# Kernel optimization log

Measured on AMD Instinct MI355X. Metric: run time of the kernel, lower is better.

Reference implementation:

```python
import jax, jax.numpy as jnp
import numpy as np

B, CHAR_LEN, LSTM, VOCAB, NATTN = 4096, 64, 400, 73, 10

def _lstm_cell(x, h, c, W_ih, W_hh, b):
    # gates: [B, 4*LSTM] in (i, f, g, o) order, matching torch.nn.LSTMCell
    g = x @ W_ih.T + h @ W_hh.T + b
    i, f, gg, o = jnp.split(g, 4, axis=1)
    i = jax.nn.sigmoid(i); f = jax.nn.sigmoid(f)
    gg = jnp.tanh(gg); o = jax.nn.sigmoid(o)
    c_new = f * c + i * gg
    h_new = o * jnp.tanh(c_new)
    return h_new, c_new

def setup_inputs() -> dict:
    key = jax.random.key(0)
    ks = jax.random.split(key, 24)
    d = {}
    d['inputs'] = jax.random.normal(ks[0], (B, 3), jnp.float32)
    for n, k in zip(['h1','c1','h2','c2','h3','c3'], ks[1:7]):
        d[n] = jax.random.normal(k, (B, LSTM), jnp.float32) * 0.1
    d['kappa'] = jax.random.uniform(ks[7], (B, NATTN), jnp.float32) * 5.0
    d['w_prev'] = jax.random.uniform(ks[8], (B, VOCAB), jnp.float32)
    d['attention_values'] = jax.random.uniform(ks[9], (B, CHAR_LEN, VOCAB), jnp.float32)
    d['attention_lengths'] = jax.random.randint(ks[10], (B,), 1, CHAR_LEN + 1, jnp.int32)
    s = 0.05
    in1 = VOCAB + 3              # lstm1 input: [w, inputs]
    in23 = 3 + LSTM + VOCAB      # lstm2/3 input: [inputs, h, w]
    attn_in = VOCAB + 3 + LSTM
    d['W_ih1'] = jax.random.normal(ks[11], (4 * LSTM, in1), jnp.float32) * s
    d['W_hh1'] = jax.random.normal(ks[12], (4 * LSTM, LSTM), jnp.float32) * s
    d['b1'] = jax.random.normal(ks[13], (4 * LSTM,), jnp.float32) * s
    d['W_attn'] = jax.random.normal(ks[14], (3 * NATTN, attn_in), jnp.float32) * s
    d['b_attn'] = jax.random.normal(ks[15], (3 * NATTN,), jnp.float32) * s
    d['W_ih2'] = jax.random.normal(ks[16], (4 * LSTM, in23), jnp.float32) * s
    d['W_hh2'] = jax.random.normal(ks[17], (4 * LSTM, LSTM), jnp.float32) * s
    d['b2'] = jax.random.normal(ks[18], (4 * LSTM,), jnp.float32) * s
    d['W_ih3'] = jax.random.normal(ks[19], (4 * LSTM, in23), jnp.float32) * s
    d['W_hh3'] = jax.random.normal(ks[20], (4 * LSTM, LSTM), jnp.float32) * s
    d['b3'] = jax.random.normal(ks[21], (4 * LSTM,), jnp.float32) * s
    return d

def reference(inputs, h1, c1, h2, c2, h3, c3, kappa, w_prev, attention_values,
              attention_lengths, W_ih1, W_hh1, b1, W_attn, b_attn,
              W_ih2, W_hh2, b2, W_ih3, W_hh3, b3):
    char_len = attention_values.shape[1]
    # --- LSTM 1 ---
    s1_in = jnp.concatenate([w_prev, inputs], axis=1)
    h1n, c1n = _lstm_cell(s1_in, h1, c1, W_ih1, W_hh1, b1)
    # --- Gaussian-mixture location attention ---
    attn_in = jnp.concatenate([w_prev, inputs, h1n], axis=1)
    attn_params = jax.nn.softplus(attn_in @ W_attn.T + b_attn)
    alpha, beta, kap = jnp.split(attn_params, 3, axis=1)
    kap = kappa + kap / 25.0
    beta = jnp.maximum(beta, 0.01)
    u = jnp.arange(char_len, dtype=jnp.float32)[None, None, :]           # [1,1,C]
    phi = jnp.sum(alpha[:, :, None] *
                  jnp.exp(-jnp.square(kap[:, :, None] - u) / beta[:, :, None]),
                  axis=1)                                                 # [B,C]
    seq_mask = (jnp.arange(char_len)[None, :] < attention_lengths[:, None]).astype(jnp.float32)
    w = jnp.einsum('bc,bcv->bv', phi * seq_mask, attention_values)        # [B,V]
    # --- LSTM 2 & 3 ---
    s2_in = jnp.concatenate([inputs, h1n, w], axis=1)
    h2n, c2n = _lstm_cell(s2_in, h2, c2, W_ih2, W_hh2, b2)
    s3_in = jnp.concatenate([inputs, h2n, w], axis=1)
    h3n, c3n = _lstm_cell(s3_in, h3, c3, W_ih3, W_hh3, b3)
    return h3n
```

## Files before the change

kernel.cpp:

```cpp
#include <hip/hip_runtime.h>
#include <hip/hip_bf16.h>


#define B_SZ     4096
#define LSTM_N   400
#define NG       1600
#define VOCAB    73
#define NATTN    10
#define CHARLEN  64
#define KP1      512
#define KP23     896

typedef _Float16 half8 __attribute__((ext_vector_type(8)));
typedef __attribute__((ext_vector_type(4))) float floatx4;

__device__ __forceinline__ void gload_lds16(const void* g, void* l) {
    __builtin_amdgcn_global_load_lds(
        (const __attribute__((address_space(1))) void*)g,
        (__attribute__((address_space(3))) void*)l, 16, 0, 0);
}

__device__ __forceinline__ int lds_off(int r, int g) {
    return (r << 6) + ((((g ^ r) & 7)) << 3);
}

#define CW1   102400
#define CW23  179200
#define CWA   4096
#define CX1   262144
#define CXA   57344
#define CX23  253952
#define O1    (CW1)
#define O2    (O1 + CW23)
#define O3    (O2 + CW23)
#define O4    (O3 + CWA)
#define O5    (O4 + CX1)
#define O6    (O5 + CXA)
#define O7    (O6 + CX23)

__global__ __launch_bounds__(256) void pack_all(const float* __restrict__ Wih1,
                                                const float* __restrict__ Whh1,
                                                const float* __restrict__ Wih2,
                                                const float* __restrict__ Whh2,
                                                const float* __restrict__ Wih3,
                                                const float* __restrict__ Whh3,
                                                const float* __restrict__ W_attn,
                                                const float* __restrict__ w_prev,
                                                const float* __restrict__ inputs,
                                                const float* __restrict__ h1,
                                                const float* __restrict__ h2,
                                                const float* __restrict__ h3,
                                                _Float16* __restrict__ W1,
                                                _Float16* __restrict__ W2,
                                                _Float16* __restrict__ W3,
                                                _Float16* __restrict__ Wa,
                                                _Float16* __restrict__ X1,
                                                _Float16* __restrict__ XA,
                                                _Float16* __restrict__ X2,
                                                _Float16* __restrict__ X3)
{
    const int id = blockIdx.x * 256 + threadIdx.x;
    half8 hv;

    if (id < O1) {
        const int row = id >> 6;
        const int k0  = (id & 63) << 3;
        const int u = row >> 2, g = row & 3;
        const int src = g * 400 + u;
#pragma unroll
        for (int e = 0; e < 8; e++) {
            const int k = k0 + e;
            float x = 0.f;
            if (k < 76)           x = Wih1[(size_t)src * 76 + k];
            else if (k < 476)     x = Whh1[(size_t)src * 400 + (k - 76)];
            hv[e] = (_Float16)x;
        }
        *(half8*)(W1 + (size_t)row * KP1 + k0) = hv;
    } else if (id < O3) {
        const int id2 = id - O1;
        const bool is3 = (id2 >= CW23);
        const int id3 = is3 ? id2 - CW23 : id2;
        const int row = id3 / 112;
        const int k0  = (id3 - row * 112) << 3;
        const int u = row >> 2, g = row & 3;
        const int src = g * 400 + u;
        const float* Wih = is3 ? Wih3 : Wih2;
        const float* Whh = is3 ? Whh3 : Whh2;
#pragma unroll
        for (int e = 0; e < 8; e++) {
            const int k = k0 + e;
            float x = 0.f;
            if (k < 400)          x = Wih[(size_t)src * 476 + 3 + k];
            else if (k < 403)     x = Wih[(size_t)src * 476 + (k - 400)];
            else if (k < 476)     x = Wih[(size_t)src * 476 + k];
            else if (k < 876)     x = Whh[(size_t)src * 400 + (k - 476)];
            hv[e] = (_Float16)x;
        }
        *(half8*)((is3 ? W3 : W2) + (size_t)row * KP23 + k0) = hv;
    } else if (id < O4) {
        const int id4 = id - O3;
        const int row = id4 >> 6;
        const int k0  = (id4 & 63) << 3;
#pragma unroll
        for (int e = 0; e < 8; e++) {
            const int k = k0 + e;
            float x = 0.f;
            if (row < 30) {
                if (k < 400)      x = W_attn[(size_t)row * 476 + 76 + k];
                else if (k < 473) x = W_attn[(size_t)row * 476 + (k - 400)];
                else if (k < 476) x = W_attn[(size_t)row * 476 + 73 + (k - 473)];
            }
            hv[e] = (_Float16)x;
        }
        *(half8*)(Wa + (size_t)row * KP1 + k0) = hv;
    } else if (id < O5) {
        const int id5 = id - O4;
        const int b  = id5 >> 6;
        const int k0 = (id5 & 63) << 3;
#pragma unroll
        for (int e = 0; e < 8; e++) {
            const int k = k0 + e;
            float x = 0.f;
            if (k < 73)           x = w_prev[(size_t)b * 73 + k];
            else if (k < 76)      x = inputs[(size_t)b * 3 + (k - 73)];
            else if (k < 476)     x = h1[(size_t)b * 400 + (k - 76)];
            hv[e] = (_Float16)x;
        }
        *(half8*)(X1 + (size_t)b * KP1 + k0) = hv;
    } else if (id < O6) {
        const int id6 = id - O5;
        const int b  = id6 / 14;
        const int k0 = 400 + ((id6 - b * 14) << 3);
#pragma unroll
        for (int e = 0; e < 8; e++) {
            const int k = k0 + e;
            float x = 0.f;
            if (k < 473)          x = w_prev[(size_t)b * 73 + (k - 400)];
            else if (k < 476)     x = inputs[(size_t)b * 3 + (k - 473)];
            hv[e] = (_Float16)x;
        }
        *(half8*)(XA + (size_t)b * KP1 + k0) = hv;
    } else if (id < O7) {
        const int id7 = id - O6;
        const int b  = id7 / 62;
        const int k0 = 400 + ((id7 - b * 62) << 3);
        half8 h2v, h3v;
#pragma unroll
        for (int e = 0; e < 8; e++) {
            const int k = k0 + e;
            float x2 = 0.f, x3 = 0.f;
            if (k < 403)                    { x2 = inputs[(size_t)b * 3 + (k - 400)]; x3 = x2; }
            else if (k >= 476 && k < 876)   { x2 = h2[(size_t)b * 400 + (k - 476)];
                                              x3 = h3[(size_t)b * 400 + (k - 476)]; }
            h2v[e] = (_Float16)x2;
            h3v[e] = (_Float16)x3;
        }
        *(half8*)(X2 + (size_t)b * KP23 + k0) = h2v;
        *(half8*)(X3 + (size_t)b * KP23 + k0) = h3v;
    }
}

template<int KP>
__global__ __launch_bounds__(256) void gemm_fused_t(const _Float16* __restrict__ Wm,
                                                    const _Float16* __restrict__ X,
                                                    const float* __restrict__ bias,
                                                    const float* __restrict__ c_in,
                                                    _Float16* __restrict__ d1, int ld1,
                                                    _Float16* __restrict__ d2, int ld2,
                                                    float* __restrict__ fout)
{
    __shared__ _Float16 As[2][64 * 64];
    __shared__ _Float16 Bs[2][128 * 64];

    const int t    = threadIdx.x;
    const int w    = t >> 6;
    const int lane = t & 63;
    const int quad = lane >> 4;
    const int l16  = lane & 15;
    const int m0   = blockIdx.y * 64;
    const int n0   = blockIdx.x * 128;
    const int wm   = (w >> 1) * 32;
    const int wn   = (w & 1) * 64;
    const int lr   = lane >> 3;
    const int gq   = (lane & 7) ^ lr;

    floatx4 acc[2][4] = {};

    auto stage = [&](int sb, int k0) {
        const int cr = w * 16;
#pragma unroll
        for (int s = 0; s < 2; s++)
            gload_lds16(Wm + (size_t)(m0 + cr + s * 8 + lr) * KP + k0 + gq * 8,
                        &As[sb][(cr + s * 8) * 64]);
#pragma unroll
        for (int j = 0; j < 2; j++) {
            const int cr2 = (j * 4 + w) * 16;
#pragma unroll
            for (int s = 0; s < 2; s++)
                gload_lds16(X + (size_t)(n0 + cr2 + s * 8 + lr) * KP + k0 + gq * 8,
                            &Bs[sb][(cr2 + s * 8) * 64]);
        }
    };

    stage(0, 0);
    constexpr int NT = KP / 64;
#pragma unroll
    for (int kt = 0; kt < NT; kt++) {
        const int sb = kt & 1;
        if (kt + 1 < NT) {
            stage(sb ^ 1, (kt + 1) * 64);
            asm volatile("s_waitcnt vmcnt(6)" ::: "memory");
        } else {
            asm volatile("s_waitcnt vmcnt(0)" ::: "memory");
        }
        __builtin_amdgcn_s_barrier();
        __builtin_amdgcn_sched_barrier(0);

#pragma unroll
        for (int h = 0; h < 2; h++) {
            half8 af[2], bf[4];
#pragma unroll
            for (int i = 0; i < 2; i++)
                af[i] = *(const half8*)(&As[sb][lds_off(wm + i * 16 + l16, h * 4 + quad)]);
#pragma unroll
            for (int i = 0; i < 4; i++)
                bf[i] = *(const half8*)(&Bs[sb][lds_off(wn + i * 16 + l16, h * 4 + quad)]);
            __builtin_amdgcn_s_setprio(1);
#pragma unroll
            for (int mt = 0; mt < 2; mt++)
#pragma unroll
                for (int nt = 0; nt < 4; nt++)
                    acc[mt][nt] = __builtin_amdgcn_mfma_f32_16x16x32_f16(
                        af[mt], bf[nt], acc[mt][nt], 0, 0, 0);
            __builtin_amdgcn_s_setprio(0);
        }
        __builtin_amdgcn_s_barrier();
    }
    __builtin_amdgcn_sched_barrier(0);

    const int u0 = m0 >> 2;
    float*    Cs   = (float*)(&Bs[0][0]);
    _Float16* Hs16 = (_Float16*)(&As[0][0]);
    float*    Hs32 = (float*)(&As[0][0]);
    {
        const int bl = t >> 1;
        const int j0 = (t & 1) * 2;
#pragma unroll
        for (int j = 0; j < 2; j++) {
            floatx4 cv = *(const floatx4*)(c_in + (size_t)(n0 + bl) * LSTM_N
                                           + u0 + (j0 + j) * 4);
            *(floatx4*)(Cs + bl * 20 + (j0 + j) * 4) = cv;
        }
    }
    __syncthreads();

#pragma unroll
    for (int mt = 0; mt < 2; mt++) {
        const int ul = (wm >> 2) + mt * 4 + quad;
        const int u  = u0 + ul;
        const float bi  = bias[u];
        const float bff = bias[400 + u];
        const float bg  = bias[800 + u];
        const float bo  = bias[1200 + u];
#pragma unroll
        for (int nt = 0; nt < 4; nt++) {
            const int bl = wn + nt * 16 + l16;
            float gi = acc[mt][nt][0] + bi;
            float gf = acc[mt][nt][1] + bff;
            float gg = acc[mt][nt][2] + bg;
            float go = acc[mt][nt][3] + bo;
            float si = 1.f / (1.f + expf(-gi));
            float sf = 1.f / (1.f + expf(-gf));
            float so = 1.f / (1.f + expf(-go));
            float cn = sf * Cs[bl * 20 + ul] + si * tanhf(gg);
            float h  = so * tanhf(cn);
            if (fout) Hs32[bl * 20 + ul] = h;
            else      Hs16[bl * 24 + ul] = (_Float16)h;
        }
    }
    __syncthreads();

    if (fout) {
        const int bl = t >> 1;
        const int p0 = (t & 1) * 2;
#pragma unroll
        for (int j = 0; j < 2; j++) {
            floatx4 hvv = *(const floatx4*)(Hs32 + bl * 20 + (p0 + j) * 4);
            *(floatx4*)(fout + (size_t)(n0 + bl) * LSTM_N + u0 + (p0 + j) * 4) = hvv;
        }
    } else {
        const int bl = t >> 1;
        const int p  = t & 1;
        half8 hvv = *(const half8*)(Hs16 + bl * 24 + p * 8);
        *(half8*)(d1 + (size_t)(n0 + bl) * ld1 + u0 + p * 8) = hvv;
        if (d2) *(half8*)(d2 + (size_t)(n0 + bl) * ld2 + u0 + p * 8) = hvv;
    }
}

__global__ __launch_bounds__(256) void attn_fused(const _Float16* __restrict__ Wa,
                                                  const _Float16* __restrict__ XA,
                                                  const float* __restrict__ b_attn,
                                                  const float* __restrict__ kappa,
                                                  const float* __restrict__ AV,
                                                  const int* __restrict__ alen,
                                                  _Float16* __restrict__ X2,
                                                  _Float16* __restrict__ X3)
{
    __shared__ _Float16 Wa_s[30 * KP1];
    __shared__ float prm[4][32];
    __shared__ float phi_s[4][CHARLEN];

    const int t = threadIdx.x;
#pragma unroll
    for (int i = 0; i < 8; i++) {
        const int idx = t + i * 256;
        if (idx < 1920) {
            const int row = idx >> 6;
            const int c8  = (idx & 63) << 3;
            *(half8*)(&Wa_s[row * KP1 + c8]) = *(const half8*)(Wa + (size_t)row * KP1 + c8);
        }
    }
    __syncthreads();

    const int wave = t >> 6;
    const int lane = t & 63;
    const int b = blockIdx.x * 4 + wave;

    half8 xa = *(const half8*)(XA + (size_t)b * KP1 + lane * 8);
    float xf[8];
#pragma unroll
    for (int e = 0; e < 8; e++) xf[e] = (float)xa[e];

    float myp = 0.f;
#pragma unroll
    for (int m = 0; m < 30; m++) {
        half8 wv = *(const half8*)(&Wa_s[m * KP1 + lane * 8]);
        float s = 0.f;
#pragma unroll
        for (int e = 0; e < 8; e++) s += (float)wv[e] * xf[e];
#pragma unroll
        for (int sh = 32; sh >= 1; sh >>= 1) s += __shfl_xor(s, sh, 64);
        if (lane == m) myp = s;
    }

    if (lane < 30) {
        float p  = myp + b_attn[lane];
        float sp = (p > 20.f) ? p : log1pf(expf(p));
        float v;
        if (lane < 10)      v = sp;
        else if (lane < 20) v = fmaxf(sp, 0.01f);
        else                v = kappa[(size_t)b * NATTN + (lane - 20)] + sp * (1.f / 25.f);
        prm[wave][lane] = v;
    }
    __syncthreads();

    const int len = alen[b];
    {
        int c = lane;
        float phi = 0.f;
#pragma unroll
        for (int j = 0; j < NATTN; j++) {
            float d = prm[wave][20 + j] - (float)c;
            phi += prm[wave][j] * expf(-d * d / prm[wave][10 + j]);
        }
        phi_s[wave][c] = (c < len) ? phi : 0.f;
    }
    __syncthreads();

    for (int v0 = 0; v0 < VOCAB; v0 += 64) {
        const int v = v0 + lane;
        if (v < VOCAB) {
            const float* avb = AV + (size_t)b * CHARLEN * VOCAB + v;
            float s = 0.f;
            for (int c = 0; c < len; c++)
                s += phi_s[wave][c] * avb[(size_t)c * VOCAB];
            _Float16 wv = (_Float16)s;
            X2[(size_t)b * KP23 + 403 + v] = wv;
            X3[(size_t)b * KP23 + 403 + v] = wv;
        }
    }
}

extern "C" void kernel_launch(void* const* d_in, const int* in_sizes, int n_in,
                              void* d_out, int out_size, void* d_ws, size_t ws_size,
                              hipStream_t stream)
{
    const float* inputs = (const float*)d_in[0];
    const float* h1     = (const float*)d_in[1];
    const float* c1     = (const float*)d_in[2];
    const float* h2     = (const float*)d_in[3];
    const float* c2     = (const float*)d_in[4];
    const float* h3     = (const float*)d_in[5];
    const float* c3     = (const float*)d_in[6];
    const float* kappa  = (const float*)d_in[7];
    const float* w_prev = (const float*)d_in[8];
    const float* AV     = (const float*)d_in[9];
    const int*   alen   = (const int*)d_in[10];
    const float* W_ih1  = (const float*)d_in[11];
    const float* W_hh1  = (const float*)d_in[12];
    const float* b1     = (const float*)d_in[13];
    const float* W_attn = (const float*)d_in[14];
    const float* b_attn = (const float*)d_in[15];
    const float* W_ih2  = (const float*)d_in[16];
    const float* W_hh2  = (const float*)d_in[17];
    const float* b2     = (const float*)d_in[18];
    const float* W_ih3  = (const float*)d_in[19];
    const float* W_hh3  = (const float*)d_in[20];
    const float* b3     = (const float*)d_in[21];
    float* out = (float*)d_out;

    char* p = (char*)d_ws;
    _Float16* X1 = (_Float16*)p; p += (size_t)B_SZ * KP1 * 2;
    _Float16* XA = (_Float16*)p; p += (size_t)B_SZ * KP1 * 2;
    _Float16* X2 = (_Float16*)p; p += (size_t)B_SZ * KP23 * 2;
    _Float16* X3 = (_Float16*)p; p += (size_t)B_SZ * KP23 * 2;
    _Float16* W1 = (_Float16*)p; p += (size_t)NG * KP1 * 2;
    _Float16* W2 = (_Float16*)p; p += (size_t)NG * KP23 * 2;
    _Float16* W3 = (_Float16*)p; p += (size_t)NG * KP23 * 2;
    _Float16* Wa = (_Float16*)p; p += (size_t)64 * KP1 * 2;

    pack_all<<<O7 / 256, 256, 0, stream>>>(W_ih1, W_hh1, W_ih2, W_hh2,
                                           W_ih3, W_hh3, W_attn,
                                           w_prev, inputs, h1, h2, h3,
                                           W1, W2, W3, Wa, X1, XA, X2, X3);

    const dim3 fgrid(B_SZ / 128, NG / 64);

    gemm_fused_t<KP1><<<fgrid, 256, 0, stream>>>(W1, X1, b1, c1,
                                                 XA, KP1, X2, KP23, nullptr);
    attn_fused<<<B_SZ / 4, 256, 0, stream>>>(Wa, XA, b_attn, kappa, AV, alen, X2, X3);
    gemm_fused_t<KP23><<<fgrid, 256, 0, stream>>>(W2, X2, b2, c2,
                                                  X3, KP23, nullptr, 0, nullptr);
    gemm_fused_t<KP23><<<fgrid, 256, 0, stream>>>(W3, X3, b3, c3,
                                                  nullptr, 0, nullptr, 0, out);
}
```

Baseline: 298.9 us.

## Enlarge fused LSTM GEMM tiles to 128x256 with 512 threads and XCD-aware block remap

Each gate GEMM block now computes a 128-gate-row by 256-batch tile using 8 waves, each holding a 4x4 set of MFMA accumulators. The gate dimension is padded from 1600 to 1664 so it divides into 13 tiles, with zero-filled weights and masking of the invalid units in the epilogue. Block IDs are also remapped so that consecutive work items are spread across the 8 XCDs. The aim is more operand reuse per LDS load and fewer global reloads of weights and activations. In exchange the kernel does about 4% padded work, launches only 208 blocks on a 256-CU device, and uses more registers per thread.

```diff
diff --git a/kernel.cpp b/kernel.cpp
--- a/kernel.cpp
+++ b/kernel.cpp
@@ -4,7 +4,8 @@
 
 #define B_SZ     4096
 #define LSTM_N   400
-#define NG       1600
+#define MPAD     1664
+#define MT       13
 #define VOCAB    73
 #define NATTN    10
 #define CHARLEN  64
@@ -24,8 +25,8 @@
     return (r << 6) + ((((g ^ r) & 7)) << 3);
 }
 
-#define CW1   102400
-#define CW23  179200
+#define CW1   106496
+#define CW23  186368
 #define CWA   4096
 #define CX1   262144
 #define CXA   57344
@@ -71,8 +72,10 @@
         for (int e = 0; e < 8; e++) {
             const int k = k0 + e;
             float x = 0.f;
-            if (k < 76)           x = Wih1[(size_t)src * 76 + k];
-            else if (k < 476)     x = Whh1[(size_t)src * 400 + (k - 76)];
+            if (u < 400) {
+                if (k < 76)           x = Wih1[(size_t)src * 76 + k];
+                else if (k < 476)     x = Whh1[(size_t)src * 400 + (k - 76)];
+            }
             hv[e] = (_Float16)x;
         }
         *(half8*)(W1 + (size_t)row * KP1 + k0) = hv;
@@ -90,10 +93,12 @@
         for (int e = 0; e < 8; e++) {
             const int k = k0 + e;
             float x = 0.f;
-            if (k < 400)          x = Wih[(size_t)src * 476 + 3 + k];
-            else if (k < 403)     x = Wih[(size_t)src * 476 + (k - 400)];
-            else if (k < 476)     x = Wih[(size_t)src * 476 + k];
-            else if (k < 876)     x = Whh[(size_t)src * 400 + (k - 476)];
+            if (u < 400) {
+                if (k < 400)          x = Wih[(size_t)src * 476 + 3 + k];
+                else if (k < 403)     x = Wih[(size_t)src * 476 + (k - 400)];
+                else if (k < 476)     x = Wih[(size_t)src * 476 + k];
+                else if (k < 876)     x = Whh[(size_t)src * 400 + (k - 476)];
+            }
             hv[e] = (_Float16)x;
         }
         *(half8*)((is3 ? W3 : W2) + (size_t)row * KP23 + k0) = hv;
@@ -161,7 +166,7 @@
 }
 
 template<int KP>
-__global__ __launch_bounds__(256) void gemm_fused_t(const _Float16* __restrict__ Wm,
+__global__ __launch_bounds__(512) void gemm_fused_t(const _Float16* __restrict__ Wm,
                                                     const _Float16* __restrict__ X,
                                                     const float* __restrict__ bias,
                                                     const float* __restrict__ c_in,
@@ -169,37 +174,35 @@
                                                     _Float16* __restrict__ d2, int ld2,
                                                     float* __restrict__ fout)
 {
-    __shared__ _Float16 As[2][64 * 64];
-    __shared__ _Float16 Bs[2][128 * 64];
+    __shared__ _Float16 lds[2][(128 + 256) * 64];
 
     const int t    = threadIdx.x;
     const int w    = t >> 6;
     const int lane = t & 63;
     const int quad = lane >> 4;
     const int l16  = lane & 15;
-    const int m0   = blockIdx.y * 64;
-    const int n0   = blockIdx.x * 128;
-    const int wm   = (w >> 1) * 32;
-    const int wn   = (w & 1) * 64;
+    const int fid  = blockIdx.y * 16 + blockIdx.x;
+    const int work = (fid & 7) * 26 + (fid >> 3);
+    const int bx   = work / MT;
+    const int by   = work - bx * MT;
+    const int m0   = by * 128;
+    const int n0   = bx * 256;
+    const int wm   = (w >> 2) * 64;
+    const int wn   = (w & 3) * 64;
     const int lr   = lane >> 3;
     const int gq   = (lane & 7) ^ lr;
 
-    floatx4 acc[2][4] = {};
+    floatx4 acc[4][4] = {};
 
     auto stage = [&](int sb, int k0) {
-        const int cr = w * 16;
 #pragma unroll
         for (int s = 0; s < 2; s++)
-            gload_lds16(Wm + (size_t)(m0 + cr + s * 8 + lr) * KP + k0 + gq * 8,
-                        &As[sb][(cr + s * 8) * 64]);
-#pragma unroll
-        for (int j = 0; j < 2; j++) {
-            const int cr2 = (j * 4 + w) * 16;
-#pragma unroll
-            for (int s = 0; s < 2; s++)
-                gload_lds16(X + (size_t)(n0 + cr2 + s * 8 + lr) * KP + k0 + gq * 8,
-                            &Bs[sb][(cr2 + s * 8) * 64]);
-        }
+            gload_lds16(Wm + (size_t)(m0 + w * 16 + s * 8 + lr) * KP + k0 + gq * 8,
+                        &lds[sb][(w * 16 + s * 8) * 64]);
+#pragma unroll
+        for (int s = 0; s < 4; s++)
+            gload_lds16(X + (size_t)(n0 + w * 32 + s * 8 + lr) * KP + k0 + gq * 8,
+                        &lds[sb][(128 + w * 32 + s * 8) * 64]);
     };
 
     stage(0, 0);
@@ -218,16 +221,16 @@
 
 #pragma unroll
         for (int h = 0; h < 2; h++) {
-            half8 af[2], bf[4];
-#pragma unroll
-            for (int i = 0; i < 2; i++)
-                af[i] = *(const half8*)(&As[sb][lds_off(wm + i * 16 + l16, h * 4 + quad)]);
+            half8 af[4], bf[4];
 #pragma unroll
             for (int i = 0; i < 4; i++)
-                bf[i] = *(const half8*)(&Bs[sb][lds_off(wn + i * 16 + l16, h * 4 + quad)]);
+                af[i] = *(const half8*)(&lds[sb][lds_off(wm + i * 16 + l16, h * 4 + quad)]);
+#pragma unroll
+            for (int i = 0; i < 4; i++)
+                bf[i] = *(const half8*)(&lds[sb][lds_off(128 + wn + i * 16 + l16, h * 4 + quad)]);
             __builtin_amdgcn_s_setprio(1);
 #pragma unroll
-            for (int mt = 0; mt < 2; mt++)
+            for (int mt = 0; mt < 4; mt++)
 #pragma unroll
                 for (int nt = 0; nt < 4; nt++)
                     acc[mt][nt] = __builtin_amdgcn_mfma_f32_16x16x32_f16(
@@ -238,30 +241,34 @@
     }
     __builtin_amdgcn_sched_barrier(0);
 
-    const int u0 = m0 >> 2;
-    float*    Cs   = (float*)(&Bs[0][0]);
-    _Float16* Hs16 = (_Float16*)(&As[0][0]);
-    float*    Hs32 = (float*)(&As[0][0]);
+    const int u0     = by * 32;
+    const int nvalid = (u0 + 32 <= LSTM_N) ? 32 : (LSTM_N - u0);
+    float*    Cs   = (float*)&lds[0][0];
+    _Float16* Hs16 = (_Float16*)&lds[1][0];
+    float*    Hs32 = (float*)&lds[1][0];
     {
         const int bl = t >> 1;
-        const int j0 = (t & 1) * 2;
-#pragma unroll
-        for (int j = 0; j < 2; j++) {
-            floatx4 cv = *(const floatx4*)(c_in + (size_t)(n0 + bl) * LSTM_N
-                                           + u0 + (j0 + j) * 4);
-            *(floatx4*)(Cs + bl * 20 + (j0 + j) * 4) = cv;
+        const int j0 = (t & 1) * 16;
+#pragma unroll
+        for (int j = 0; j < 4; j++) {
+            const int ulc = j0 + j * 4;
+            if (ulc < nvalid) {
+                floatx4 cv = *(const floatx4*)(c_in + (size_t)(n0 + bl) * LSTM_N + u0 + ulc);
+                *(floatx4*)(Cs + bl * 36 + ulc) = cv;
+            }
         }
     }
     __syncthreads();
 
 #pragma unroll
-    for (int mt = 0; mt < 2; mt++) {
+    for (int mt = 0; mt < 4; mt++) {
         const int ul = (wm >> 2) + mt * 4 + quad;
         const int u  = u0 + ul;
-        const float bi  = bias[u];
-        const float bff = bias[400 + u];
-        const float bg  = bias[800 + u];
-        const float bo  = bias[1200 + u];
+        const bool uv = ul < nvalid;
+        const float bi  = uv ? bias[u] : 0.f;
+        const float bff = uv ? bias[400 + u] : 0.f;
+        const float bg  = uv ? bias[800 + u] : 0.f;
+        const float bo  = uv ? bias[1200 + u] : 0.f;
 #pragma unroll
         for (int nt = 0; nt < 4; nt++) {
             const int bl = wn + nt * 16 + l16;
@@ -272,28 +279,38 @@
             float si = 1.f / (1.f + expf(-gi));
             float sf = 1.f / (1.f + expf(-gf));
             float so = 1.f / (1.f + expf(-go));
-            float cn = sf * Cs[bl * 20 + ul] + si * tanhf(gg);
+            float cn = sf * Cs[bl * 36 + ul] + si * tanhf(gg);
             float h  = so * tanhf(cn);
-            if (fout) Hs32[bl * 20 + ul] = h;
-            else      Hs16[bl * 24 + ul] = (_Float16)h;
+            if (uv) {
+                if (fout) Hs32[bl * 36 + ul] = h;
+                else      Hs16[bl * 40 + ul] = (_Float16)h;
+            }
         }
     }
     __syncthreads();
 
     if (fout) {
         const int bl = t >> 1;
-        const int p0 = (t & 1) * 2;
-#pragma unroll
-        for (int j = 0; j < 2; j++) {
-            floatx4 hvv = *(const floatx4*)(Hs32 + bl * 20 + (p0 + j) * 4);
-            *(floatx4*)(fout + (size_t)(n0 + bl) * LSTM_N + u0 + (p0 + j) * 4) = hvv;
+        const int j0 = (t & 1) * 16;
+#pragma unroll
+        for (int j = 0; j < 4; j++) {
+            const int ulc = j0 + j * 4;
+            if (ulc < nvalid)
+                *(floatx4*)(fout + (size_t)(n0 + bl) * LSTM_N + u0 + ulc) =
+                    *(const floatx4*)(Hs32 + bl * 36 + ulc);
         }
     } else {
         const int bl = t >> 1;
-        const int p  = t & 1;
-        half8 hvv = *(const half8*)(Hs16 + bl * 24 + p * 8);
-        *(half8*)(d1 + (size_t)(n0 + bl) * ld1 + u0 + p * 8) = hvv;
-        if (d2) *(half8*)(d2 + (size_t)(n0 + bl) * ld2 + u0 + p * 8) = hvv;
+        const int j0 = (t & 1) * 16;
+#pragma unroll
+        for (int j = 0; j < 2; j++) {
+            const int ulc = j0 + j * 8;
+            if (ulc < nvalid) {
+                half8 hvv = *(const half8*)(Hs16 + bl * 40 + ulc);
+                *(half8*)(d1 + (size_t)(n0 + bl) * ld1 + u0 + ulc) = hvv;
+                if (d2) *(half8*)(d2 + (size_t)(n0 + bl) * ld2 + u0 + ulc) = hvv;
+            }
+        }
     }
 }
 
@@ -414,9 +431,9 @@
     _Float16* XA = (_Float16*)p; p += (size_t)B_SZ * KP1 * 2;
     _Float16* X2 = (_Float16*)p; p += (size_t)B_SZ * KP23 * 2;
     _Float16* X3 = (_Float16*)p; p += (size_t)B_SZ * KP23 * 2;
-    _Float16* W1 = (_Float16*)p; p += (size_t)NG * KP1 * 2;
-    _Float16* W2 = (_Float16*)p; p += (size_t)NG * KP23 * 2;
-    _Float16* W3 = (_Float16*)p; p += (size_t)NG * KP23 * 2;
+    _Float16* W1 = (_Float16*)p; p += (size_t)MPAD * KP1 * 2;
+    _Float16* W2 = (_Float16*)p; p += (size_t)MPAD * KP23 * 2;
+    _Float16* W3 = (_Float16*)p; p += (size_t)MPAD * KP23 * 2;
     _Float16* Wa = (_Float16*)p; p += (size_t)64 * KP1 * 2;
 
     pack_all<<<O7 / 256, 256, 0, stream>>>(W_ih1, W_hh1, W_ih2, W_hh2,
@@ -424,13 +441,13 @@
                                            w_prev, inputs, h1, h2, h3,
                                            W1, W2, W3, Wa, X1, XA, X2, X3);
 
-    const dim3 fgrid(B_SZ / 128, NG / 64);
-
-    gemm_fused_t<KP1><<<fgrid, 256, 0, stream>>>(W1, X1, b1, c1,
+    const dim3 fgrid(B_SZ / 256, MT);
+
+    gemm_fused_t<KP1><<<fgrid, 512, 0, stream>>>(W1, X1, b1, c1,
                                                  XA, KP1, X2, KP23, nullptr);
     attn_fused<<<B_SZ / 4, 256, 0, stream>>>(Wa, XA, b_attn, kappa, AV, alen, X2, X3);
-    gemm_fused_t<KP23><<<fgrid, 256, 0, stream>>>(W2, X2, b2, c2,
+    gemm_fused_t<KP23><<<fgrid, 512, 0, stream>>>(W2, X2, b2, c2,
                                                   X3, KP23, nullptr, 0, nullptr);
-    gemm_fused_t<KP23><<<fgrid, 256, 0, stream>>>(W3, X3, b3, c3,
+    gemm_fused_t<KP23><<<fgrid, 512, 0, stream>>>(W3, X3, b3, c3,
                                                   nullptr, 0, nullptr, 0, out);
 }
```

Measured after the change: 295.6 us. No clear change (-1.1%).

## Triple-buffer GEMM LDS stages and remap blocks for XCD-local reuse

Applied to the files above, without the earlier changes.

The fused LSTM GEMM moves from a double-buffered to a triple-buffered LDS pipeline, prefetching two K-tiles ahead with adjusted vmcnt waits so more global loads are in flight. Tiles are merged into one LDS array per stage. The block index is also remapped so each of the 8 XCDs gets a contiguous set of 4 batch-column tiles across all 25 gate rows. This is meant to improve L2 reuse of the activation tiles. LDS use per block rises to 72KB, which may cut occupancy.

```diff
diff --git a/kernel.cpp b/kernel.cpp
--- a/kernel.cpp
+++ b/kernel.cpp
@@ -169,16 +169,20 @@
                                                     _Float16* __restrict__ d2, int ld2,
                                                     float* __restrict__ fout)
 {
-    __shared__ _Float16 As[2][64 * 64];
-    __shared__ _Float16 Bs[2][128 * 64];
+    __shared__ _Float16 lds[3][192 * 64];
 
     const int t    = threadIdx.x;
     const int w    = t >> 6;
     const int lane = t & 63;
     const int quad = lane >> 4;
     const int l16  = lane & 15;
-    const int m0   = blockIdx.y * 64;
-    const int n0   = blockIdx.x * 128;
+    const int fid  = blockIdx.y * 32 + blockIdx.x;
+    const int xcd  = fid & 7;
+    const int loc  = fid >> 3;
+    const int bx   = xcd * 4 + loc / 25;
+    const int by   = loc % 25;
+    const int m0   = by * 64;
+    const int n0   = bx * 128;
     const int wm   = (w >> 1) * 32;
     const int wn   = (w & 1) * 64;
     const int lr   = lane >> 3;
@@ -187,28 +191,26 @@
     floatx4 acc[2][4] = {};
 
     auto stage = [&](int sb, int k0) {
-        const int cr = w * 16;
 #pragma unroll
         for (int s = 0; s < 2; s++)
-            gload_lds16(Wm + (size_t)(m0 + cr + s * 8 + lr) * KP + k0 + gq * 8,
-                        &As[sb][(cr + s * 8) * 64]);
-#pragma unroll
-        for (int j = 0; j < 2; j++) {
-            const int cr2 = (j * 4 + w) * 16;
-#pragma unroll
-            for (int s = 0; s < 2; s++)
-                gload_lds16(X + (size_t)(n0 + cr2 + s * 8 + lr) * KP + k0 + gq * 8,
-                            &Bs[sb][(cr2 + s * 8) * 64]);
-        }
+            gload_lds16(Wm + (size_t)(m0 + w * 16 + s * 8 + lr) * KP + k0 + gq * 8,
+                        &lds[sb][(w * 16 + s * 8) * 64]);
+#pragma unroll
+        for (int s = 0; s < 4; s++)
+            gload_lds16(X + (size_t)(n0 + w * 32 + s * 8 + lr) * KP + k0 + gq * 8,
+                        &lds[sb][(64 + w * 32 + s * 8) * 64]);
     };
 
     stage(0, 0);
+    stage(1, 64);
     constexpr int NT = KP / 64;
 #pragma unroll
     for (int kt = 0; kt < NT; kt++) {
-        const int sb = kt & 1;
-        if (kt + 1 < NT) {
-            stage(sb ^ 1, (kt + 1) * 64);
+        const int sb = kt % 3;
+        if (kt + 2 < NT) {
+            stage((kt + 2) % 3, (kt + 2) * 64);
+            asm volatile("s_waitcnt vmcnt(12)" ::: "memory");
+        } else if (kt + 1 < NT) {
             asm volatile("s_waitcnt vmcnt(6)" ::: "memory");
         } else {
             asm volatile("s_waitcnt vmcnt(0)" ::: "memory");
@@ -221,10 +223,10 @@
             half8 af[2], bf[4];
 #pragma unroll
             for (int i = 0; i < 2; i++)
-                af[i] = *(const half8*)(&As[sb][lds_off(wm + i * 16 + l16, h * 4 + quad)]);
+                af[i] = *(const half8*)(&lds[sb][lds_off(wm + i * 16 + l16, h * 4 + quad)]);
 #pragma unroll
             for (int i = 0; i < 4; i++)
-                bf[i] = *(const half8*)(&Bs[sb][lds_off(wn + i * 16 + l16, h * 4 + quad)]);
+                bf[i] = *(const half8*)(&lds[sb][lds_off(64 + wn + i * 16 + l16, h * 4 + quad)]);
             __builtin_amdgcn_s_setprio(1);
 #pragma unroll
             for (int mt = 0; mt < 2; mt++)
@@ -239,9 +241,9 @@
     __builtin_amdgcn_sched_barrier(0);
 
     const int u0 = m0 >> 2;
-    float*    Cs   = (float*)(&Bs[0][0]);
-    _Float16* Hs16 = (_Float16*)(&As[0][0]);
-    float*    Hs32 = (float*)(&As[0][0]);
+    float*    Cs   = (float*)&lds[0][0];
+    _Float16* Hs16 = (_Float16*)&lds[1][0];
+    float*    Hs32 = (float*)&lds[1][0];
     {
         const int bl = t >> 1;
         const int j0 = (t & 1) * 2;
@@ -424,7 +426,7 @@
                                            w_prev, inputs, h1, h2, h3,
                                            W1, W2, W3, Wa, X1, XA, X2, X3);
 
-    const dim3 fgrid(B_SZ / 128, NG / 64);
+    const dim3 fgrid(32, 25);
 
     gemm_fused_t<KP1><<<fgrid, 256, 0, stream>>>(W1, X1, b1, c1,
                                                  XA, KP1, X2, KP23, nullptr);
```

New measurement: 289.7 us. 3.1% less time.
